# Kernel optimization log

Hardware: AMD Instinct MI355X
Metric: run time of the kernel (lower is better)

## Reference

```python
import jax, jax.numpy as jnp
import numpy as np

B, T, S, A4 = 64, 4096, 305, 4

def setup_inputs() -> dict:
    key = jax.random.key(0)
    k1, k2, k3, k4 = jax.random.split(key, 4)
    obs = jax.random.randint(k1, (B, T), 0, A4)
    inputs = jax.nn.one_hot(obs, A4, dtype=jnp.float32)          # [B,T,4] one-hot nucleotides
    init_kernel = jax.random.normal(k2, (S,), dtype=jnp.float32)
    transition_kernel = jax.random.normal(k3, (S, S), dtype=jnp.float32)
    emission_kernel = jax.random.normal(k4, (S, A4), dtype=jnp.float32)
    return {"inputs": inputs, "init_kernel": init_kernel,
            "transition_kernel": transition_kernel, "emission_kernel": emission_kernel}

def reference(inputs, init_kernel, transition_kernel, emission_kernel):
    # Kernels -> stochastic matrices (row softmax), as in CgpHmmCell.
    I = jax.nn.softmax(init_kernel)                   # [S]
    A = jax.nn.softmax(transition_kernel, axis=-1)    # [S,S]
    Bm = jax.nn.softmax(emission_kernel, axis=-1)     # [S,4]
    # Per-step emission likelihoods E[b,t,s] = B[s, obs_t] (one-hot contraction).
    E = jnp.einsum('bta,sa->bts', inputs, Bm)         # [B,T,S]
    # t = 0
    a0 = I[None, :] * E[:, 0]                         # [B,S]
    s0 = jnp.sum(a0, axis=-1, keepdims=True)
    alpha0 = a0 / s0
    ll0 = jnp.log(s0[:, 0])                           # [B]

    def step(carry, e_t):
        alpha, ll = carry                             # alpha [B,S], ll [B]; e_t [B,S]
        a = (alpha @ A) * e_t                         # scaled alpha recursion
        s = jnp.sum(a, axis=-1, keepdims=True)
        alpha = a / s
        return (alpha, ll + jnp.log(s[:, 0])), alpha

    E_rest = jnp.moveaxis(E[:, 1:], 1, 0)             # time-major [T-1,B,S]
    (alpha_T, loglik), _alpha_seq = jax.lax.scan(step, (alpha0, ll0), E_rest)
    return loglik                                     # loglik_state [B]
```

## Files before the change

kernel.cpp:

```cpp
#include <hip/hip_runtime.h>


constexpr int NS  = 305;
constexpr int NSP = 320;
constexpr int NT  = 4096;
constexpr int NW  = 8;
constexpr int RPW = 40;
constexpr int CPT = 5;
constexpr int NORM_MASK = 7;

__global__ __launch_bounds__(512, 2)
void hmm_fwd(const float* __restrict__ inputs,
             const float* __restrict__ initk,
             const float* __restrict__ transk,
             const float* __restrict__ emisk,
             float* __restrict__ out)
{
    __shared__ float sBm[4 * NSP];
    __shared__ float sI[NSP];
    __shared__ float sRowsum[NSP];
    __shared__ unsigned char sObs[NT];
    __shared__ float sPart[2][NW * NSP];
    __shared__ float sN[16];

    const int tid = threadIdx.x;
    const int w   = tid >> 6;
    const int l   = tid & 63;
    const int b   = blockIdx.x;

    for (int i = tid; i < 4 * NSP; i += 512) sBm[i] = 0.f;
    for (int i = tid; i < NSP;     i += 512) sI[i]  = 0.f;
    __syncthreads();

    const float4* oh = (const float4*)(inputs + (size_t)b * NT * 4);
    #pragma unroll
    for (int i = 0; i < NT / 512; ++i) {
        int t = tid + i * 512;
        float4 v = oh[t];
        sObs[t] = (unsigned char)(int)(v.y + 2.f * v.z + 3.f * v.w + 0.5f);
    }

    if (tid < NS) {
        float4 ek = ((const float4*)emisk)[tid];
        float e0 = __expf(ek.x), e1 = __expf(ek.y), e2 = __expf(ek.z), e3 = __expf(ek.w);
        float inv = 1.f / (e0 + e1 + e2 + e3);
        sBm[0 * NSP + tid] = e0 * inv;
        sBm[1 * NSP + tid] = e1 * inv;
        sBm[2 * NSP + tid] = e2 * inv;
        sBm[3 * NSP + tid] = e3 * inv;
    }

    if (tid < NS) sI[tid] = __expf(initk[tid]);

    for (int j = 0; j < RPW; ++j) {
        int r = w + j * NW;
        float part = 0.f;
        if (r < NS) {
            #pragma unroll
            for (int k = 0; k < CPT; ++k) {
                int c = l + 64 * k;
                if (c < NS) part += __expf(transk[r * NS + c]);
            }
        }
        #pragma unroll
        for (int off = 32; off; off >>= 1) part += __shfl_xor(part, off, 64);
        if (l == 0) sRowsum[r] = part;
    }
    __syncthreads();

    float v0 = (tid < NSP) ? sI[tid] : 0.f;
    #pragma unroll
    for (int off = 32; off; off >>= 1) v0 += __shfl_xor(v0, off, 64);
    if (l == 0) sN[w] = v0;
    __syncthreads();
    float z = 0.f;
    #pragma unroll
    for (int i = 0; i < 8; ++i) z += sN[i];
    const float logZI = __logf(z);
    __syncthreads();

    float areg[RPW][CPT];
    #pragma unroll
    for (int j = 0; j < RPW; ++j) {
        const int row = w * RPW + j;
        const float invr = (row < NS) ? 1.f / sRowsum[row] : 0.f;
        #pragma unroll
        for (int k = 0; k < CPT; ++k) {
            const int col = l + 64 * k;
            float v = 0.f;
            if (row < NS && col < NS)
                v = __expf(transk[row * NS + col]) * invr;
            areg[j][k] = v;
        }
    }

    float va = 0.f;
    {
        int o0 = sObs[0];
        int col = w * RPW + l;
        if (l < RPW) va = sI[col] * sBm[o0 * NSP + col];
    }
    float ll = 0.f;

    for (int t = 1; t < NT; ++t) {
        const int o = sObs[t];
        const float ecol = (l < RPW) ? sBm[o * NSP + w * RPW + l] : 0.f;

        float acc[CPT] = {0.f, 0.f, 0.f, 0.f, 0.f};
        #pragma unroll
        for (int j = 0; j < RPW; ++j) {
            float sa = __uint_as_float(
                __builtin_amdgcn_readlane(__float_as_uint(va), j));
            #pragma unroll
            for (int k = 0; k < CPT; ++k)
                acc[k] = fmaf(sa, areg[j][k], acc[k]);
        }

        float* pb = sPart[t & 1];
        #pragma unroll
        for (int k = 0; k < CPT; ++k)
            pb[w * NSP + l + 64 * k] = acc[k];
        __syncthreads();

        if (l < RPW) {
            const int col = w * RPW + l;
            float s8 = 0.f;
            #pragma unroll
            for (int ww = 0; ww < NW; ++ww) s8 += pb[ww * NSP + col];
            va = s8 * ecol;
        } else {
            va = 0.f;
        }

        if ((t & NORM_MASK) == NORM_MASK) {
            float v = (l < RPW) ? va : 0.f;
            #pragma unroll
            for (int off = 32; off; off >>= 1) v += __shfl_xor(v, off, 64);
            const int nb = (t >> 3) & 1;
            if (l == 0) sN[nb * 8 + w] = v;
            __syncthreads();
            float tot = 0.f;
            #pragma unroll
            for (int i = 0; i < 8; ++i) tot += sN[nb * 8 + i];
            ll += __logf(tot);
            va *= 1.f / tot;
        }
    }

    if (tid == 0) out[b] = ll - logZI;
}

extern "C" void kernel_launch(void* const* d_in, const int* in_sizes, int n_in,
                              void* d_out, int out_size, void* d_ws, size_t ws_size,
                              hipStream_t stream) {
    const float* inputs = (const float*)d_in[0];
    const float* initk  = (const float*)d_in[1];
    const float* transk = (const float*)d_in[2];
    const float* emisk  = (const float*)d_in[3];
    hipLaunchKernelGGL(hmm_fwd, dim3(64), dim3(512), 0, stream,
                       inputs, initk, transk, emisk, (float*)d_out);
}
```

Before: 5.001 ms.

## Pack transition matrix to fp16 pairs, use dot2 and LDS atomics

A separate prep kernel row-normalizes the transition matrix and packs pairs of rows into half2 words in workspace. The main kernel keeps the matrix in registers at half the footprint and uses fdot2 instead of scalar FMAs. It replaces the per-wave partial-sum buffer with LDS atomic adds into a double-buffered column vector. Normalization now runs every step through a deferred sqrt-scaling scheme on the previous step's sums, which removes one barrier per step. The cost is fp16 precision in both the transition weights and the alpha vector, plus atomic contention in LDS.

```diff
diff --git a/kernel.cpp b/kernel.cpp
--- a/kernel.cpp
+++ b/kernel.cpp
@@ -1,27 +1,71 @@
 #include <hip/hip_runtime.h>
-
-
-constexpr int NS  = 305;
-constexpr int NSP = 320;
-constexpr int NT  = 4096;
-constexpr int NW  = 8;
-constexpr int RPW = 40;
-constexpr int CPT = 5;
-constexpr int NORM_MASK = 7;
+#include <hip/hip_fp16.h>
+
+
+constexpr int NS   = 305;
+constexpr int NSP  = 320;
+constexpr int NT   = 4096;
+constexpr int NW   = 8;
+constexpr int RPW  = 40;
+constexpr int NPAIR = 20;
+
+typedef _Float16 h2 __attribute__((ext_vector_type(2)));
+
+__device__ __forceinline__ float fdot2f(h2 a, h2 b, float c) {
+#if __has_builtin(__builtin_amdgcn_fdot2)
+    return __builtin_amdgcn_fdot2(a, b, c, false);
+#else
+    return c + (float)a[0] * (float)b[0] + (float)a[1] * (float)b[1];
+#endif
+}
+
+__device__ __forceinline__ float wave_sum(float v) {
+    #pragma unroll
+    for (int off = 32; off; off >>= 1) v += __shfl_xor(v, off, 64);
+    return v;
+}
+
+#define TWENTY(X) X(0) X(1) X(2) X(3) X(4) X(5) X(6) X(7) X(8) X(9) \
+  X(10) X(11) X(12) X(13) X(14) X(15) X(16) X(17) X(18) X(19)
+
+__global__ __launch_bounds__(64)
+void prep_Ah(const float* __restrict__ transk, unsigned* __restrict__ wsH)
+{
+    const int p = blockIdx.x;
+    const int l = threadIdx.x;
+    const int r0 = 2 * p, r1 = 2 * p + 1;
+    float e0[5], e1[5];
+    float s0 = 0.f, s1 = 0.f;
+    #pragma unroll
+    for (int k = 0; k < 5; ++k) {
+        const int c = l + 64 * k;
+        e0[k] = (r0 < NS && c < NS) ? __expf(transk[r0 * NS + c]) : 0.f;
+        e1[k] = (r1 < NS && c < NS) ? __expf(transk[r1 * NS + c]) : 0.f;
+        s0 += e0[k]; s1 += e1[k];
+    }
+    s0 = wave_sum(s0); s1 = wave_sum(s1);
+    const float i0 = (r0 < NS) ? 1.f / s0 : 0.f;
+    const float i1 = (r1 < NS) ? 1.f / s1 : 0.f;
+    #pragma unroll
+    for (int k = 0; k < 5; ++k) {
+        unsigned h0 = __half_as_ushort(__float2half(e0[k] * i0));
+        unsigned h1 = __half_as_ushort(__float2half(e1[k] * i1));
+        wsH[p * NSP + l + 64 * k] = h0 | (h1 << 16);
+    }
+}
 
 __global__ __launch_bounds__(512, 2)
 void hmm_fwd(const float* __restrict__ inputs,
              const float* __restrict__ initk,
-             const float* __restrict__ transk,
              const float* __restrict__ emisk,
+             const unsigned* __restrict__ wsH,
              float* __restrict__ out)
 {
     __shared__ float sBm[4 * NSP];
     __shared__ float sI[NSP];
-    __shared__ float sRowsum[NSP];
+    __shared__ float buf[2 * NSP];
+    __shared__ __align__(16) float sN[16];
     __shared__ unsigned char sObs[NT];
-    __shared__ float sPart[2][NW * NSP];
-    __shared__ float sN[16];
 
     const int tid = threadIdx.x;
     const int w   = tid >> 6;
@@ -29,7 +73,8 @@
     const int b   = blockIdx.x;
 
     for (int i = tid; i < 4 * NSP; i += 512) sBm[i] = 0.f;
-    for (int i = tid; i < NSP;     i += 512) sI[i]  = 0.f;
+    if (tid < NSP) sI[tid] = 0.f;
+    for (int i = tid; i < 2 * NSP; i += 512) buf[i] = 0.f;
     __syncthreads();
 
     const float4* oh = (const float4*)(inputs + (size_t)b * NT * 4);
@@ -48,51 +93,50 @@
         sBm[1 * NSP + tid] = e1 * inv;
         sBm[2 * NSP + tid] = e2 * inv;
         sBm[3 * NSP + tid] = e3 * inv;
-    }
-
-    if (tid < NS) sI[tid] = __expf(initk[tid]);
-
-    for (int j = 0; j < RPW; ++j) {
-        int r = w + j * NW;
-        float part = 0.f;
-        if (r < NS) {
-            #pragma unroll
-            for (int k = 0; k < CPT; ++k) {
-                int c = l + 64 * k;
-                if (c < NS) part += __expf(transk[r * NS + c]);
-            }
-        }
-        #pragma unroll
-        for (int off = 32; off; off >>= 1) part += __shfl_xor(part, off, 64);
-        if (l == 0) sRowsum[r] = part;
+        sI[tid] = __expf(initk[tid]);
     }
     __syncthreads();
 
     float v0 = (tid < NSP) ? sI[tid] : 0.f;
-    #pragma unroll
-    for (int off = 32; off; off >>= 1) v0 += __shfl_xor(v0, off, 64);
+    v0 = wave_sum(v0);
     if (l == 0) sN[w] = v0;
     __syncthreads();
-    float z = 0.f;
-    #pragma unroll
-    for (int i = 0; i < 8; ++i) z += sN[i];
-    const float logZI = __logf(z);
-    __syncthreads();
-
-    float areg[RPW][CPT];
-    #pragma unroll
-    for (int j = 0; j < RPW; ++j) {
-        const int row = w * RPW + j;
-        const float invr = (row < NS) ? 1.f / sRowsum[row] : 0.f;
-        #pragma unroll
-        for (int k = 0; k < CPT; ++k) {
-            const int col = l + 64 * k;
-            float v = 0.f;
-            if (row < NS && col < NS)
-                v = __expf(transk[row * NS + col]) * invr;
-            areg[j][k] = v;
-        }
-    }
+    float lz2;
+    {
+        const float4* s4 = (const float4*)sN;
+        float4 p0 = s4[0], p1 = s4[1];
+        lz2 = __builtin_amdgcn_logf(((p0.x + p0.y) + (p0.z + p0.w)) +
+                                    ((p1.x + p1.y) + (p1.z + p1.w)));
+    }
+    __syncthreads();
+
+    const unsigned* wh = wsH + (size_t)(w * NPAIR) * NSP + l;
+#define DECLA(J) unsigned au##J##_0, au##J##_1, au##J##_2, au##J##_3, au##J##_4;
+    TWENTY(DECLA)
+#undef DECLA
+#define LOADA(J) \
+    au##J##_0 = wh[J * NSP];        \
+    au##J##_1 = wh[J * NSP + 64];   \
+    au##J##_2 = wh[J * NSP + 128];  \
+    au##J##_3 = wh[J * NSP + 192];  \
+    au##J##_4 = wh[J * NSP + 256];
+    TWENTY(LOADA)
+#undef LOADA
+#define PINA(J) asm volatile("" : "+v"(au##J##_0), "+v"(au##J##_1), \
+    "+v"(au##J##_2), "+v"(au##J##_3), "+v"(au##J##_4));
+    TWENTY(PINA)
+#undef PINA
+
+#define DOTJ(J) { \
+    unsigned s0_ = __builtin_amdgcn_readlane(__float_as_uint(va), 2 * J);     \
+    unsigned s1_ = __builtin_amdgcn_readlane(__float_as_uint(va), 2 * J + 1); \
+    h2 sa_ = __builtin_bit_cast(h2, \
+        __builtin_amdgcn_cvt_pkrtz(__uint_as_float(s0_), __uint_as_float(s1_))); \
+    acc0 = fdot2f(sa_, __builtin_bit_cast(h2, au##J##_0), acc0); \
+    acc1 = fdot2f(sa_, __builtin_bit_cast(h2, au##J##_1), acc1); \
+    acc2 = fdot2f(sa_, __builtin_bit_cast(h2, au##J##_2), acc2); \
+    acc3 = fdot2f(sa_, __builtin_bit_cast(h2, au##J##_3), acc3); \
+    acc4 = fdot2f(sa_, __builtin_bit_cast(h2, au##J##_4), acc4); }
 
     float va = 0.f;
     {
@@ -100,54 +144,71 @@
         int col = w * RPW + l;
         if (l < RPW) va = sI[col] * sBm[o0 * NSP + col];
     }
-    float ll = 0.f;
-
-    for (int t = 1; t < NT; ++t) {
-        const int o = sObs[t];
-        const float ecol = (l < RPW) ? sBm[o * NSP + w * RPW + l] : 0.f;
-
-        float acc[CPT] = {0.f, 0.f, 0.f, 0.f, 0.f};
-        #pragma unroll
-        for (int j = 0; j < RPW; ++j) {
-            float sa = __uint_as_float(
-                __builtin_amdgcn_readlane(__float_as_uint(va), j));
-            #pragma unroll
-            for (int k = 0; k < CPT; ++k)
-                acc[k] = fmaf(sa, areg[j][k], acc[k]);
-        }
-
-        float* pb = sPart[t & 1];
-        #pragma unroll
-        for (int k = 0; k < CPT; ++k)
-            pb[w * NSP + l + 64 * k] = acc[k];
+    { float v = wave_sum(va); if (l == 0) sN[0 * 8 + w] = v; }
+    float ll2 = 0.f;
+    __syncthreads();
+
+    {
+        float acc0 = 0.f, acc1 = 0.f, acc2 = 0.f, acc3 = 0.f, acc4 = 0.f;
+        TWENTY(DOTJ)
+        atomicAdd(&buf[NSP + l      ], acc0);
+        atomicAdd(&buf[NSP + l +  64], acc1);
+        atomicAdd(&buf[NSP + l + 128], acc2);
+        atomicAdd(&buf[NSP + l + 192], acc3);
+        atomicAdd(&buf[NSP + l + 256], acc4);
         __syncthreads();
-
+        const int o = sObs[1];
         if (l < RPW) {
             const int col = w * RPW + l;
-            float s8 = 0.f;
-            #pragma unroll
-            for (int ww = 0; ww < NW; ++ww) s8 += pb[ww * NSP + col];
-            va = s8 * ecol;
-        } else {
-            va = 0.f;
+            float g = buf[NSP + col];
+            buf[NSP + col] = 0.f;
+            va = g * sBm[o * NSP + col];
+        } else va = 0.f;
+        float v = wave_sum(va);
+        if (l == 0) sN[8 + w] = v;
+    }
+
+    #pragma unroll 2
+    for (int t = 2; t < NT; ++t) {
+        const int sl = (t & 1) * NSP;
+        const int sn = (t & 1) * 8;
+        {
+            const float4* s4 = (const float4*)(sN + sn);
+            float4 p0 = s4[0], p1 = s4[1];
+            float tot = ((p0.x + p0.y) + (p0.z + p0.w)) + ((p1.x + p1.y) + (p1.z + p1.w));
+            tot = fmaxf(tot, 1e-30f);
+            ll2 += 0.5f * __builtin_amdgcn_logf(tot);
+            va  *= __frsqrt_rn(tot);
         }
-
-        if ((t & NORM_MASK) == NORM_MASK) {
-            float v = (l < RPW) ? va : 0.f;
-            #pragma unroll
-            for (int off = 32; off; off >>= 1) v += __shfl_xor(v, off, 64);
-            const int nb = (t >> 3) & 1;
-            if (l == 0) sN[nb * 8 + w] = v;
-            __syncthreads();
-            float tot = 0.f;
-            #pragma unroll
-            for (int i = 0; i < 8; ++i) tot += sN[nb * 8 + i];
-            ll += __logf(tot);
-            va *= 1.f / tot;
-        }
-    }
-
-    if (tid == 0) out[b] = ll - logZI;
+        float acc0 = 0.f, acc1 = 0.f, acc2 = 0.f, acc3 = 0.f, acc4 = 0.f;
+        TWENTY(DOTJ)
+        atomicAdd(&buf[sl + l      ], acc0);
+        atomicAdd(&buf[sl + l +  64], acc1);
+        atomicAdd(&buf[sl + l + 128], acc2);
+        atomicAdd(&buf[sl + l + 192], acc3);
+        atomicAdd(&buf[sl + l + 256], acc4);
+        __syncthreads();
+        const int o = sObs[t];
+        if (l < RPW) {
+            const int col = w * RPW + l;
+            float g = buf[sl + col];
+            buf[sl + col] = 0.f;
+            va = g * sBm[o * NSP + col];
+        } else va = 0.f;
+        float v = wave_sum(va);
+        if (l == 0) sN[sn + w] = v;
+    }
+
+    __syncthreads();
+    {
+        const float4* s4 = (const float4*)(sN + ((NT - 1) & 1) * 8);
+        float4 p0 = s4[0], p1 = s4[1];
+        float tot = ((p0.x + p0.y) + (p0.z + p0.w)) + ((p1.x + p1.y) + (p1.z + p1.w));
+        tot = fmaxf(tot, 1e-30f);
+        ll2 += __builtin_amdgcn_logf(tot);
+    }
+    if (tid == 0) out[b] = (ll2 - lz2) * 0.6931471805599453f;
+#undef DOTJ
 }
 
 extern "C" void kernel_launch(void* const* d_in, const int* in_sizes, int n_in,
@@ -157,6 +218,9 @@
     const float* initk  = (const float*)d_in[1];
     const float* transk = (const float*)d_in[2];
     const float* emisk  = (const float*)d_in[3];
+    unsigned* wsH = (unsigned*)d_ws;
+
+    hipLaunchKernelGGL(prep_Ah, dim3(NSP / 2), dim3(64), 0, stream, transk, wsH);
     hipLaunchKernelGGL(hmm_fwd, dim3(64), dim3(512), 0, stream,
-                       inputs, initk, transk, emisk, (float*)d_out);
-}
+                       inputs, initk, emisk, wsH, (float*)d_out);
+}
```

New measurement: 15.94 ms. 219% more time.
